# Kernel optimization log

Measured on AMD Instinct MI355X. Metric: run time of the kernel, lower is better.

The kernel has to match this reference:

```python
import jax, jax.numpy as jnp
import numpy as np

N = 1024      # number of atoms
L = 64        # latent_size
VOCAB = 20    # vocab_size (len(ATOM_CATEGORIES))


def _lin(key, fan_in, fan_out):
    # mimic torch nn.Linear init: U(-1/sqrt(fan_in), 1/sqrt(fan_in))
    kw, kb = jax.random.split(key)
    s = 1.0 / np.sqrt(fan_in)
    W = jax.random.uniform(kw, (fan_in, fan_out), minval=-s, maxval=s, dtype=jnp.float32)
    b = jax.random.uniform(kb, (fan_out,), minval=-s, maxval=s, dtype=jnp.float32)
    return W, b


def setup_inputs() -> dict:
    key = jax.random.key(0)
    ks = jax.random.split(key, 9)
    We1, be1 = _lin(ks[3], 2 * L + 1, L)   # mlp_e layer 1
    We2, be2 = _lin(ks[4], L, L)           # mlp_e layer 2
    Wh1, bh1 = _lin(ks[5], L + 1, L)       # mlp_h layer 1
    Wh2, bh2 = _lin(ks[6], L, L)           # mlp_h layer 2
    Wo, bo = _lin(ks[7], L, 1)             # output_mlp
    return {
        "atom_categories": jax.random.randint(ks[0], (N,), 0, VOCAB),
        "atom_coordinates": jax.random.normal(ks[1], (N, 3), dtype=jnp.float32),
        "learnable_matrix": jax.random.normal(ks[2], (VOCAB, L), dtype=jnp.float32),
        "We1": We1, "be1": be1, "We2": We2, "be2": be2,
        "Wh1": Wh1, "bh1": bh1, "Wh2": Wh2, "bh2": bh2,
        "Wo": Wo, "bo": bo,
    }


def reference(atom_categories, atom_coordinates, learnable_matrix,
              We1, be1, We2, be2, Wh1, bh1, Wh2, bh2, Wo, bo):
    Z = atom_coordinates
    # init_H: learnable_matrix.T @ one_hot(cat) == row gather
    H = learnable_matrix[atom_categories]                       # [N, L]

    # pairwise squared distances ||Z_i - Z_j||^2
    d2 = jnp.sum((Z[:, None, :] - Z[None, :, :]) ** 2, axis=-1)  # [N, N]

    # mlp_e layer 1 on concat(H_i, H_j, d2): split We1 to avoid materializing concat
    W1i, W1j, w1z = We1[:L], We1[L:2 * L], We1[2 * L]            # [L,L],[L,L],[L]
    pre_i = H @ W1i                                              # [N, L]
    pre_j = H @ W1j                                              # [N, L]
    h1 = jnp.tanh(pre_i[:, None, :] + pre_j[None, :, :]
                  + d2[:, :, None] * w1z + be1)                  # [N, N, L]
    W_e = jnp.tanh(h1 @ We2 + be2)                               # [N, N, L]

    # V[i] = sum over j != i of sum_l W_e[i,j,l]
    total = jnp.sum(W_e, axis=(1, 2))                            # [N]
    diag = jnp.einsum('iil->i', W_e)                             # [N]
    V = total - diag                                             # [N]

    # mlp_h on concat(H_i, V_i): split Wh1
    hh = jnp.tanh(H @ Wh1[:L] + V[:, None] * Wh1[L] + bh1)       # [N, L]
    newH = jnp.tanh(hh @ Wh2 + bh2)                              # [N, L]

    Hsum = jnp.sum(newH, axis=0)                                 # [L]
    return (Hsum @ Wo + bo)[0]                                   # scalar
```

## Files before the change

kernel.cpp:

```cpp
#include <hip/hip_runtime.h>
#include <hip/hip_bf16.h>


#define N_ATOMS 1024
#define L_DIM 64
#define CSCALE 2.8853900817779268f

typedef _Float16 f16x8 __attribute__((ext_vector_type(8)));
typedef __fp16  fp16x2 __attribute__((ext_vector_type(2)));
typedef float f32x4 __attribute__((ext_vector_type(4)));

__device__ __forceinline__ float tanh_fast(float x) {
    float e = __builtin_amdgcn_exp2f(x * CSCALE);
    float r = __builtin_amdgcn_rcpf(e + 1.0f);
    return fmaf(-2.0f, r, 1.0f);
}

__global__ __launch_bounds__(256) void k_prep(const int* __restrict__ cat,
                                              const float* __restrict__ LM,
                                              const float* __restrict__ We1,
                                              const float* __restrict__ be1,
                                              const float* __restrict__ We2,
                                              const float* __restrict__ be2,
                                              float* __restrict__ H,
                                              float* __restrict__ preI,
                                              float* __restrict__ P3,
                                              float* __restrict__ Vpart,
                                              f16x8* __restrict__ bHg,
                                              f16x8* __restrict__ bLg,
                                              float* __restrict__ biasg,
                                              float* __restrict__ out) {
    int t = threadIdx.x;
    int sub = t >> 6, l = t & 63;
    int i = blockIdx.x * 4 + sub;
    if (blockIdx.x == 0 && t == 0) out[0] = 0.f;
    if (t < 4) Vpart[blockIdx.x * 4 + t] = 0.f;
    __shared__ float hrow[4][L_DIM];
    float hv = LM[cat[i] * L_DIM + l];
    hrow[sub][l] = hv;
    H[i * L_DIM + l] = hv;
    __syncthreads();
    float s1 = 0.f, s2 = 0.f;
#pragma unroll
    for (int m = 0; m < L_DIM; m++) {
        float h = hrow[sub][m];
        s1 = fmaf(h, We1[m * L_DIM + l], s1);
        s2 = fmaf(h, We1[(L_DIM + m) * L_DIM + l], s2);
    }
    preI[i * L_DIM + l] = s1 * CSCALE;
    int cc = i >> 4;
    int Ll = i & 15;
    int quad = (l >> 3) & 3;
    int L = quad * 16 + Ll;
    int g = ((l >> 5) << 1) | ((l >> 2) & 1);
    int e2 = l & 3;
    P3[cc * 1024 + g * 256 + L * 4 + e2] = (s2 + be1[l]) * CSCALE;

    if (blockIdx.x == 0) {
        int nt = t >> 6;
        int lane = t & 63;
        int q2 = lane >> 4, nl2 = lane & 15;
        float psum = 0.f;
#pragma unroll
        for (int kt = 0; kt < 2; kt++) {
            f16x8 hi8, lo8;
#pragma unroll
            for (int e = 0; e < 8; e++) {
                float x = We2[(kt * 32 + q2 * 8 + e) * L_DIM + nt * 16 + nl2];
                psum += x;
                float wp = -2.0f * CSCALE * x;
                _Float16 hi = (_Float16)wp;
                hi8[e] = hi;
                lo8[e] = (_Float16)(wp - (float)hi);
            }
            bHg[(kt * 4 + nt) * 64 + lane] = hi8;
            bLg[(kt * 4 + nt) * 64 + lane] = lo8;
        }
        psum += __shfl_xor(psum, 16);
        psum += __shfl_xor(psum, 32);
        biasg[lane * 4 + nt] = CSCALE * (be2[nt * 16 + nl2] + psum);
    }
}

__global__ __launch_bounds__(256) void k_main(const float* __restrict__ Z,
                                              const float* __restrict__ We1,
                                              const float* __restrict__ preI,
                                              const float* __restrict__ P3,
                                              const f16x8* __restrict__ bHg,
                                              const f16x8* __restrict__ bLg,
                                              const float* __restrict__ biasg,
                                              const float* __restrict__ H,
                                              const float* __restrict__ We2,
                                              const float* __restrict__ be2,
                                              const float* __restrict__ Wh1,
                                              const float* __restrict__ bh1,
                                              const float* __restrict__ Wh2,
                                              const float* __restrict__ bh2,
                                              const float* __restrict__ Wo,
                                              const float* __restrict__ bo,
                                              float* __restrict__ Vpart,
                                              float* __restrict__ out) {
    int bid = blockIdx.x;
    int i = bid >> 1, half = bid & 1;
    int t = threadIdx.x;
    int lane = t & 63;
    int wave = t >> 6;
    int nlo = lane & 15;
    int quad = lane >> 4;

    __shared__ float d2s[512];
    __shared__ float red[256];
    __shared__ f16x8 bLs[8 * 64];
    __shared__ float dgt[L_DIM];
    __shared__ float hrow_s[L_DIM];
    __shared__ float hhs[L_DIM];
    __shared__ float RallS;
    __shared__ int   winflag;

    float zi0 = Z[i * 3], zi1 = Z[i * 3 + 1], zi2 = Z[i * 3 + 2];
    for (int p = t; p < 512; p += 256) {
        int j = half * 512 + p;
        float a = zi0 - Z[j * 3], b = zi1 - Z[j * 3 + 1], c = zi2 - Z[j * 3 + 2];
        d2s[p] = a * a + b * b + c * c;
    }

    f32x4 aiR[4], wzR[4];
#pragma unroll
    for (int g = 0; g < 4; g++) {
        int mb = ((g >> 1) << 5) + (quad << 3) + ((g & 1) << 2);
        aiR[g] = *(const f32x4*)(preI + i * L_DIM + mb);
        f32x4 wz = *(const f32x4*)(We1 + 2 * L_DIM * L_DIM + mb);
        wzR[g] = wz * CSCALE;
    }

    f16x8 bH[4][2];
#pragma unroll
    for (int nt = 0; nt < 4; nt++) {
        bH[nt][0] = bHg[(0 * 4 + nt) * 64 + lane];
        bH[nt][1] = bHg[(1 * 4 + nt) * 64 + lane];
    }
#pragma unroll
    for (int idx = 0; idx < 2; idx++) {
        int e = wave + idx * 4;
        bLs[e * 64 + lane] = bLg[e * 64 + lane];
    }
    f32x4 bias4 = *(const f32x4*)(biasg + lane * 4);

    const float* Pbase = P3 + (half * 32 + wave * 8) * 1024 + lane * 4;
    f32x4 p0 = *(const f32x4*)(Pbase + 0 * 256) + aiR[0];
    f32x4 p1 = *(const f32x4*)(Pbase + 1 * 256) + aiR[1];
    f32x4 p2 = *(const f32x4*)(Pbase + 2 * 256) + aiR[2];
    f32x4 p3 = *(const f32x4*)(Pbase + 3 * 256) + aiR[3];

    __syncthreads();

    f32x4 Vr4 = {0.f, 0.f, 0.f, 0.f};
    for (int k = 0; k < 8; k++) {
        float d2 = d2s[(wave * 8 + k) * 16 + nlo];
        f32x4 d2v = {d2, d2, d2, d2};

        f32x4 z0 = p0 + d2v * wzR[0];
        f32x4 z1 = p1 + d2v * wzR[1];
        f32x4 z2 = p2 + d2v * wzR[2];
        f32x4 z3 = p3 + d2v * wzR[3];
        f32x4 ex0, ex1, ex2, ex3;
#pragma unroll
        for (int e = 0; e < 4; e++) {
            ex0[e] = __builtin_amdgcn_exp2f(z0[e]);
            ex1[e] = __builtin_amdgcn_exp2f(z1[e]);
            ex2[e] = __builtin_amdgcn_exp2f(z2[e]);
            ex3[e] = __builtin_amdgcn_exp2f(z3[e]);
        }
        ex0 += 1.0f; ex1 += 1.0f; ex2 += 1.0f; ex3 += 1.0f;
        f32x4 r0, r1, r2, r3;
#pragma unroll
        for (int e = 0; e < 4; e++) {
            r0[e] = __builtin_amdgcn_rcpf(ex0[e]);
            r1[e] = __builtin_amdgcn_rcpf(ex1[e]);
            r2[e] = __builtin_amdgcn_rcpf(ex2[e]);
            r3[e] = __builtin_amdgcn_rcpf(ex3[e]);
        }
        union { f16x8 v; fp16x2 h2[4]; } u0, u1;
        u0.h2[0] = __builtin_amdgcn_cvt_pkrtz(r0[0], r0[1]);
        u0.h2[1] = __builtin_amdgcn_cvt_pkrtz(r0[2], r0[3]);
        u0.h2[2] = __builtin_amdgcn_cvt_pkrtz(r1[0], r1[1]);
        u0.h2[3] = __builtin_amdgcn_cvt_pkrtz(r1[2], r1[3]);
        u1.h2[0] = __builtin_amdgcn_cvt_pkrtz(r2[0], r2[1]);
        u1.h2[1] = __builtin_amdgcn_cvt_pkrtz(r2[2], r2[3]);
        u1.h2[2] = __builtin_amdgcn_cvt_pkrtz(r3[0], r3[1]);
        u1.h2[3] = __builtin_amdgcn_cvt_pkrtz(r3[2], r3[3]);
        f16x8 aH0 = u0.v, aH1 = u1.v;

        if (k < 7) {
            const float* nb = Pbase + (k + 1) * 1024;
            p0 = *(const f32x4*)(nb + 0 * 256) + aiR[0];
            p1 = *(const f32x4*)(nb + 1 * 256) + aiR[1];
            p2 = *(const f32x4*)(nb + 2 * 256) + aiR[2];
            p3 = *(const f32x4*)(nb + 3 * 256) + aiR[3];
        }

#pragma unroll
        for (int nt = 0; nt < 4; nt++) {
            f16x8 bl0 = bLs[(0 * 4 + nt) * 64 + lane];
            f16x8 bl1 = bLs[(1 * 4 + nt) * 64 + lane];
            f32x4 acc = {bias4[nt], bias4[nt], bias4[nt], bias4[nt]};
            acc = __builtin_amdgcn_mfma_f32_16x16x32_f16(aH0, bH[nt][0], acc, 0, 0, 0);
            acc = __builtin_amdgcn_mfma_f32_16x16x32_f16(aH0, bl0, acc, 0, 0, 0);
            acc = __builtin_amdgcn_mfma_f32_16x16x32_f16(aH1, bH[nt][1], acc, 0, 0, 0);
            acc = __builtin_amdgcn_mfma_f32_16x16x32_f16(aH1, bl1, acc, 0, 0, 0);
            f32x4 ev;
#pragma unroll
            for (int r4 = 0; r4 < 4; r4++) ev[r4] = __builtin_amdgcn_exp2f(acc[r4]);
            ev += 1.0f;
            f32x4 rv;
#pragma unroll
            for (int r4 = 0; r4 < 4; r4++) rv[r4] = __builtin_amdgcn_rcpf(ev[r4]);
            Vr4 += rv;
        }
    }

    red[t] = Vr4[0] + Vr4[1] + Vr4[2] + Vr4[3];
    __syncthreads();

    if (t < 64) {
        float r = red[t] + red[t + 64] + red[t + 128] + red[t + 192];
#pragma unroll
        for (int o = 32; o > 0; o >>= 1) r += __shfl_xor(r, o);
        if (t == 0) {
            float old = atomicAdd(Vpart + i, r);
            winflag = (old != 0.0f);
            RallS = old + r;
        }
    }
    __syncthreads();

    if (winflag) {
        if (t < 64) {
            int cc = i >> 4, Ll = i & 15;
            int q2 = (t >> 3) & 3;
            int g = ((t >> 5) << 1) | ((t >> 2) & 1);
            float z = preI[i * L_DIM + t] + P3[cc * 1024 + g * 256 + (q2 * 16 + Ll) * 4 + (t & 3)];
            float rr = __builtin_amdgcn_rcpf(__builtin_amdgcn_exp2f(z) + 1.0f);
            dgt[t] = fmaf(-2.0f, rr, 1.0f);
            hrow_s[t] = H[i * L_DIM + t];
        }
        __syncthreads();
        if (t < 64) {
            float S = be2[t];
#pragma unroll
            for (int m = 0; m < L_DIM; m++) S = fmaf(dgt[m], We2[m * L_DIM + t], S);
            float rd = __builtin_amdgcn_rcpf(__builtin_amdgcn_exp2f(S * CSCALE) + 1.0f);
#pragma unroll
            for (int o = 32; o > 0; o >>= 1) rd += __shfl_xor(rd, o);
            float V = fmaf(-2.0f, RallS - rd, (float)(1023 * L_DIM));
            float s = 0.f;
#pragma unroll
            for (int m = 0; m < L_DIM; m++) s = fmaf(hrow_s[m], Wh1[m * L_DIM + t], s);
            s = fmaf(V, Wh1[L_DIM * L_DIM + t], s) + bh1[t];
            hhs[t] = tanh_fast(s);
        }
        __syncthreads();
        if (t < 64) {
            float s2 = 0.f;
#pragma unroll
            for (int m = 0; m < L_DIM; m++) s2 = fmaf(hhs[m], Wh2[m * L_DIM + t], s2);
            float nh = tanh_fast(s2 + bh2[t]);
            float w = nh * Wo[t];
#pragma unroll
            for (int o = 32; o > 0; o >>= 1) w += __shfl_down(w, o);
            if (t == 0) atomicAdd(out, w + (i == 0 ? bo[0] : 0.f));
        }
    }
}

extern "C" void kernel_launch(void* const* d_in, const int* in_sizes, int n_in,
                              void* d_out, int out_size, void* d_ws, size_t ws_size,
                              hipStream_t stream) {
    const int*   cat = (const int*)  d_in[0];
    const float* Z   = (const float*)d_in[1];
    const float* LM  = (const float*)d_in[2];
    const float* We1 = (const float*)d_in[3];
    const float* be1 = (const float*)d_in[4];
    const float* We2 = (const float*)d_in[5];
    const float* be2 = (const float*)d_in[6];
    const float* Wh1 = (const float*)d_in[7];
    const float* bh1 = (const float*)d_in[8];
    const float* Wh2 = (const float*)d_in[9];
    const float* bh2 = (const float*)d_in[10];
    const float* Wo  = (const float*)d_in[11];
    const float* bo  = (const float*)d_in[12];
    float* out = (float*)d_out;

    float* ws    = (float*)d_ws;
    float* H     = ws;
    float* preI  = H     + N_ATOMS * L_DIM;
    float* P3    = preI  + N_ATOMS * L_DIM;
    float* Vpart = P3    + N_ATOMS * L_DIM;
    float* biasg = Vpart + N_ATOMS;
    f16x8* bHg   = (f16x8*)(biasg + 256);
    f16x8* bLg   = bHg + 8 * 64;

    k_prep<<<N_ATOMS / 4, 256, 0, stream>>>(cat, LM, We1, be1, We2, be2,
                                            H, preI, P3, Vpart, bHg, bLg, biasg, out);
    k_main<<<N_ATOMS * 2, 256, 0, stream>>>(Z, We1, preI, P3, bHg, bLg, biasg,
                                            H, We2, be2, Wh1, bh1, Wh2, bh2, Wo, bo,
                                            Vpart, out);
}
```

Measured before the change: 121.7 us.

## Fuse prep and main kernels into one cooperative kernel with grid sync

Replaces the two-kernel prep/main sequence with a single cooperative kernel: one block per atom computes its own embedding row, pre-activations and d2 row, and block 0 packs the split-fp16 We2 fragments. A grid-wide barrier then separates this from the MFMA pair loop, and the per-atom mlp_h and output reduction are done in the same block. The aim is to remove the second launch and the global round-trips for H and preI, at the cost of a grid sync and the requirement that all 1024 blocks be co-resident (enforced via launch bounds with 4 blocks per CU). The old two-kernel path stays as a fallback if the cooperative launch fails. The output is accumulated with atomicAdd and the new kernel never zeroes it, so correctness depends on the output already being zeroed.

```diff
diff --git a/kernel.cpp b/kernel.cpp
--- a/kernel.cpp
+++ b/kernel.cpp
@@ -1,5 +1,7 @@
 #include <hip/hip_runtime.h>
-#include <hip/hip_bf16.h>
+#include <hip/hip_cooperative_groups.h>
+
+namespace cg = cooperative_groups;
 
 
 #define N_ATOMS 1024
@@ -14,6 +16,230 @@
     float e = __builtin_amdgcn_exp2f(x * CSCALE);
     float r = __builtin_amdgcn_rcpf(e + 1.0f);
     return fmaf(-2.0f, r, 1.0f);
+}
+
+__global__ __launch_bounds__(256, 4) void k_all(const int* __restrict__ cat,
+                                                const float* __restrict__ Z,
+                                                const float* __restrict__ LM,
+                                                const float* __restrict__ We1,
+                                                const float* __restrict__ be1,
+                                                const float* __restrict__ We2,
+                                                const float* __restrict__ be2,
+                                                const float* __restrict__ Wh1,
+                                                const float* __restrict__ bh1,
+                                                const float* __restrict__ Wh2,
+                                                const float* __restrict__ bh2,
+                                                const float* __restrict__ Wo,
+                                                const float* __restrict__ bo,
+                                                float* __restrict__ P3,
+                                                f16x8* __restrict__ bHg,
+                                                f16x8* __restrict__ bLg,
+                                                float* __restrict__ biasg,
+                                                float* __restrict__ out) {
+    int i = blockIdx.x;
+    int t = threadIdx.x;
+    int lane = t & 63;
+    int wave = t >> 6;
+    int nlo = lane & 15;
+    int quad = lane >> 4;
+
+    __shared__ __align__(16) float d2s[N_ATOMS];
+    __shared__ float red[256];
+    __shared__ f16x8 bLs[8 * 64];
+    __shared__ __align__(16) float hrow[L_DIM];
+    __shared__ __align__(16) float preIs[L_DIM];
+    __shared__ __align__(16) float prejbs[L_DIM];
+    __shared__ float dgt[L_DIM];
+    __shared__ float hhs[L_DIM];
+
+    if (t < 64) hrow[t] = LM[cat[i] * L_DIM + t];
+    float zi0 = Z[i * 3], zi1 = Z[i * 3 + 1], zi2 = Z[i * 3 + 2];
+    for (int p = t; p < N_ATOMS; p += 256) {
+        float a = zi0 - Z[p * 3], b = zi1 - Z[p * 3 + 1], c = zi2 - Z[p * 3 + 2];
+        d2s[p] = a * a + b * b + c * c;
+    }
+    __syncthreads();
+
+    if (wave == 0) {
+        float s1 = 0.f;
+#pragma unroll
+        for (int m = 0; m < L_DIM; m++) s1 = fmaf(hrow[m], We1[m * L_DIM + lane], s1);
+        preIs[lane] = s1 * CSCALE;
+    } else if (wave == 1) {
+        float s2 = 0.f;
+#pragma unroll
+        for (int m = 0; m < L_DIM; m++) s2 = fmaf(hrow[m], We1[(L_DIM + m) * L_DIM + lane], s2);
+        float v = (s2 + be1[lane]) * CSCALE;
+        prejbs[lane] = v;
+        int cc = i >> 4, Ll = i & 15;
+        int q2 = (lane >> 3) & 3;
+        int Lr = q2 * 16 + Ll;
+        int g = ((lane >> 5) << 1) | ((lane >> 2) & 1);
+        int e2 = lane & 3;
+        __builtin_nontemporal_store(v, &P3[cc * 1024 + g * 256 + Lr * 4 + e2]);
+    }
+
+    if (i == 0) {
+        int nt = wave;
+        float psum = 0.f;
+#pragma unroll
+        for (int kt = 0; kt < 2; kt++) {
+            f16x8 hi8, lo8;
+#pragma unroll
+            for (int e = 0; e < 8; e++) {
+                float x = We2[(kt * 32 + quad * 8 + e) * L_DIM + nt * 16 + nlo];
+                psum += x;
+                float wp = -2.0f * CSCALE * x;
+                _Float16 hi = (_Float16)wp;
+                hi8[e] = hi;
+                lo8[e] = (_Float16)(wp - (float)hi);
+            }
+            __builtin_nontemporal_store(hi8, &bHg[(kt * 4 + nt) * 64 + lane]);
+            __builtin_nontemporal_store(lo8, &bLg[(kt * 4 + nt) * 64 + lane]);
+        }
+        psum += __shfl_xor(psum, 16);
+        psum += __shfl_xor(psum, 32);
+        __builtin_nontemporal_store(CSCALE * (be2[nt * 16 + nlo] + psum),
+                                    &biasg[lane * 4 + nt]);
+    }
+
+    __threadfence();
+    cg::this_grid().sync();
+
+    f16x8 bH[4][2];
+#pragma unroll
+    for (int nt = 0; nt < 4; nt++) {
+        bH[nt][0] = bHg[(0 * 4 + nt) * 64 + lane];
+        bH[nt][1] = bHg[(1 * 4 + nt) * 64 + lane];
+    }
+#pragma unroll
+    for (int idx = 0; idx < 2; idx++) {
+        int e = wave + idx * 4;
+        bLs[e * 64 + lane] = bLg[e * 64 + lane];
+    }
+    f32x4 bias4 = *(const f32x4*)(biasg + lane * 4);
+
+    f32x4 aiR[4], wzR[4];
+#pragma unroll
+    for (int g = 0; g < 4; g++) {
+        int mb = ((g >> 1) << 5) + (quad << 3) + ((g & 1) << 2);
+        aiR[g] = *(const f32x4*)(preIs + mb);
+        f32x4 wz = *(const f32x4*)(We1 + 2 * L_DIM * L_DIM + mb);
+        wzR[g] = wz * CSCALE;
+    }
+
+    const float* Pbase = P3 + wave * 16 * 1024 + lane * 4;
+    f32x4 p0 = *(const f32x4*)(Pbase + 0 * 256) + aiR[0];
+    f32x4 p1 = *(const f32x4*)(Pbase + 1 * 256) + aiR[1];
+    f32x4 p2 = *(const f32x4*)(Pbase + 2 * 256) + aiR[2];
+    f32x4 p3 = *(const f32x4*)(Pbase + 3 * 256) + aiR[3];
+
+    __syncthreads();
+
+    f32x4 Vr4 = {0.f, 0.f, 0.f, 0.f};
+    for (int k = 0; k < 16; k++) {
+        float d2 = d2s[(wave * 16 + k) * 16 + nlo];
+        f32x4 d2v = {d2, d2, d2, d2};
+
+        f32x4 z0 = p0 + d2v * wzR[0];
+        f32x4 z1 = p1 + d2v * wzR[1];
+        f32x4 z2 = p2 + d2v * wzR[2];
+        f32x4 z3 = p3 + d2v * wzR[3];
+        f32x4 ex0, ex1, ex2, ex3;
+#pragma unroll
+        for (int e = 0; e < 4; e++) {
+            ex0[e] = __builtin_amdgcn_exp2f(z0[e]);
+            ex1[e] = __builtin_amdgcn_exp2f(z1[e]);
+            ex2[e] = __builtin_amdgcn_exp2f(z2[e]);
+            ex3[e] = __builtin_amdgcn_exp2f(z3[e]);
+        }
+        ex0 += 1.0f; ex1 += 1.0f; ex2 += 1.0f; ex3 += 1.0f;
+        f32x4 r0, r1, r2, r3;
+#pragma unroll
+        for (int e = 0; e < 4; e++) {
+            r0[e] = __builtin_amdgcn_rcpf(ex0[e]);
+            r1[e] = __builtin_amdgcn_rcpf(ex1[e]);
+            r2[e] = __builtin_amdgcn_rcpf(ex2[e]);
+            r3[e] = __builtin_amdgcn_rcpf(ex3[e]);
+        }
+        union { f16x8 v; fp16x2 h2[4]; } u0, u1;
+        u0.h2[0] = __builtin_amdgcn_cvt_pkrtz(r0[0], r0[1]);
+        u0.h2[1] = __builtin_amdgcn_cvt_pkrtz(r0[2], r0[3]);
+        u0.h2[2] = __builtin_amdgcn_cvt_pkrtz(r1[0], r1[1]);
+        u0.h2[3] = __builtin_amdgcn_cvt_pkrtz(r1[2], r1[3]);
+        u1.h2[0] = __builtin_amdgcn_cvt_pkrtz(r2[0], r2[1]);
+        u1.h2[1] = __builtin_amdgcn_cvt_pkrtz(r2[2], r2[3]);
+        u1.h2[2] = __builtin_amdgcn_cvt_pkrtz(r3[0], r3[1]);
+        u1.h2[3] = __builtin_amdgcn_cvt_pkrtz(r3[2], r3[3]);
+        f16x8 aH0 = u0.v, aH1 = u1.v;
+
+        if (k < 15) {
+            const float* nb = Pbase + (k + 1) * 1024;
+            p0 = *(const f32x4*)(nb + 0 * 256) + aiR[0];
+            p1 = *(const f32x4*)(nb + 1 * 256) + aiR[1];
+            p2 = *(const f32x4*)(nb + 2 * 256) + aiR[2];
+            p3 = *(const f32x4*)(nb + 3 * 256) + aiR[3];
+        }
+
+#pragma unroll
+        for (int nt = 0; nt < 4; nt++) {
+            f16x8 bl0 = bLs[(0 * 4 + nt) * 64 + lane];
+            f16x8 bl1 = bLs[(1 * 4 + nt) * 64 + lane];
+            f32x4 acc = {bias4[nt], bias4[nt], bias4[nt], bias4[nt]};
+            acc = __builtin_amdgcn_mfma_f32_16x16x32_f16(aH0, bH[nt][0], acc, 0, 0, 0);
+            acc = __builtin_amdgcn_mfma_f32_16x16x32_f16(aH0, bl0, acc, 0, 0, 0);
+            acc = __builtin_amdgcn_mfma_f32_16x16x32_f16(aH1, bH[nt][1], acc, 0, 0, 0);
+            acc = __builtin_amdgcn_mfma_f32_16x16x32_f16(aH1, bl1, acc, 0, 0, 0);
+            f32x4 ev;
+#pragma unroll
+            for (int r4 = 0; r4 < 4; r4++) ev[r4] = __builtin_amdgcn_exp2f(acc[r4]);
+            ev += 1.0f;
+            f32x4 rv;
+#pragma unroll
+            for (int r4 = 0; r4 < 4; r4++) rv[r4] = __builtin_amdgcn_rcpf(ev[r4]);
+            Vr4 += rv;
+        }
+    }
+
+    red[t] = Vr4[0] + Vr4[1] + Vr4[2] + Vr4[3];
+    __syncthreads();
+
+    float Rall;
+    if (t < 64) {
+        float r = red[t] + red[t + 64] + red[t + 128] + red[t + 192];
+#pragma unroll
+        for (int o = 32; o > 0; o >>= 1) r += __shfl_xor(r, o);
+        Rall = r;
+        float z = preIs[t] + prejbs[t];
+        float rr = __builtin_amdgcn_rcpf(__builtin_amdgcn_exp2f(z) + 1.0f);
+        dgt[t] = fmaf(-2.0f, rr, 1.0f);
+    }
+    __syncthreads();
+    if (t < 64) {
+        float S = be2[t];
+#pragma unroll
+        for (int m = 0; m < L_DIM; m++) S = fmaf(dgt[m], We2[m * L_DIM + t], S);
+        float rd = __builtin_amdgcn_rcpf(__builtin_amdgcn_exp2f(S * CSCALE) + 1.0f);
+#pragma unroll
+        for (int o = 32; o > 0; o >>= 1) rd += __shfl_xor(rd, o);
+        float V = fmaf(-2.0f, Rall - rd, (float)(1023 * L_DIM));
+        float s = 0.f;
+#pragma unroll
+        for (int m = 0; m < L_DIM; m++) s = fmaf(hrow[m], Wh1[m * L_DIM + t], s);
+        s = fmaf(V, Wh1[L_DIM * L_DIM + t], s) + bh1[t];
+        hhs[t] = tanh_fast(s);
+    }
+    __syncthreads();
+    if (t < 64) {
+        float s2 = 0.f;
+#pragma unroll
+        for (int m = 0; m < L_DIM; m++) s2 = fmaf(hhs[m], Wh2[m * L_DIM + t], s2);
+        float nh = tanh_fast(s2 + bh2[t]);
+        float w = nh * Wo[t];
+#pragma unroll
+        for (int o = 32; o > 0; o >>= 1) w += __shfl_down(w, o);
+        if (t == 0) atomicAdd(out, w + (i == 0 ? bo[0] : 0.f));
+    }
 }
 
 __global__ __launch_bounds__(256) void k_prep(const int* __restrict__ cat,
@@ -300,9 +526,18 @@
     f16x8* bHg   = (f16x8*)(biasg + 256);
     f16x8* bLg   = bHg + 8 * 64;
 
-    k_prep<<<N_ATOMS / 4, 256, 0, stream>>>(cat, LM, We1, be1, We2, be2,
-                                            H, preI, P3, Vpart, bHg, bLg, biasg, out);
-    k_main<<<N_ATOMS * 2, 256, 0, stream>>>(Z, We1, preI, P3, bHg, bLg, biasg,
-                                            H, We2, be2, Wh1, bh1, Wh2, bh2, Wo, bo,
-                                            Vpart, out);
+    void* args[] = { (void*)&cat, (void*)&Z, (void*)&LM, (void*)&We1, (void*)&be1,
+                     (void*)&We2, (void*)&be2, (void*)&Wh1, (void*)&bh1,
+                     (void*)&Wh2, (void*)&bh2, (void*)&Wo, (void*)&bo,
+                     (void*)&P3, (void*)&bHg, (void*)&bLg, (void*)&biasg,
+                     (void*)&out };
+    hipError_t rc = hipLaunchCooperativeKernel((void*)k_all, dim3(N_ATOMS), dim3(256),
+                                               args, 0, stream);
+    if (rc != hipSuccess) {
+        k_prep<<<N_ATOMS / 4, 256, 0, stream>>>(cat, LM, We1, be1, We2, be2,
+                                                H, preI, P3, Vpart, bHg, bLg, biasg, out);
+        k_main<<<N_ATOMS * 2, 256, 0, stream>>>(Z, We1, preI, P3, bHg, bLg, biasg,
+                                                H, We2, be2, Wh1, bh1, Wh2, bh2, Wo, bo,
+                                                Vpart, out);
+    }
 }
```

After: 329.3 us. +170.6%, slower.
